# Optimization experiments

Measured on AMD Instinct MI355X. Metric: run time of the kernel, lower is better.

## Reference

```python
import jax, jax.numpy as jnp
import numpy as np

B, S, H, NH, L, ML = 4, 2048, 768, 8, 128, 15
DH = H // NH
PERIOD = 16  # newline every 16 tokens -> 15 content tokens per line


def _layernorm(x, g, b, eps=1e-5):
    m = x.mean(-1, keepdims=True)
    v = ((x - m) ** 2).mean(-1, keepdims=True)
    return (x - m) / jnp.sqrt(v + eps) * g + b


def setup_inputs() -> dict:
    key = jax.random.key(0)
    ks = jax.random.split(key, 8)
    sc = 0.02
    return {
        "hidden": jax.random.normal(ks[0], (B, S, H), jnp.float32),
        "in_proj_w": jax.random.normal(ks[1], (3 * H, H), jnp.float32) * sc,
        "in_proj_b": jnp.zeros((3 * H,), jnp.float32),
        "out_proj_w": jax.random.normal(ks[2], (H, H), jnp.float32) * sc,
        "out_proj_b": jnp.zeros((H,), jnp.float32),
        "W1": jax.random.normal(ks[3], (H, 2 * H), jnp.float32) * sc,
        "b1": jnp.zeros((H,), jnp.float32),
        "g1": jnp.ones((H,), jnp.float32),
        "be1": jnp.zeros((H,), jnp.float32),
        "W2": jax.random.normal(ks[4], (H, H), jnp.float32) * sc,
        "b2": jnp.zeros((H,), jnp.float32),
        "g2": jnp.ones((H,), jnp.float32),
        "be2": jnp.zeros((H,), jnp.float32),
        "W3": jax.random.normal(ks[5], (1, H), jnp.float32) * sc,
        "b3": jnp.zeros((1,), jnp.float32),
        # padded ragged line structure (what the torch loops derive from newline positions)
        "line_starts": jnp.tile(jnp.arange(L, dtype=jnp.int32) * PERIOD, (B, 1)),  # [B,L]
        "line_lens": jnp.full((B, L), ML, jnp.int32),                              # [B,L]
        "context_len": jnp.full((B,), S, jnp.int32),                               # [B]
    }


def reference(hidden, in_proj_w, in_proj_b, out_proj_w, out_proj_b,
              W1, b1, g1, be1, W2, b2, g2, be2, W3, b3,
              line_starts, line_lens, context_len):
    # --- gather per-line tokens into a padded [B, L, ML, H] block ---
    pos = line_starts[:, :, None] + jnp.arange(ML, dtype=line_starts.dtype)      # [B,L,ML]
    tok_mask = jnp.arange(ML)[None, None, :] < line_lens[:, :, None]             # [B,L,ML]
    pos_c = jnp.clip(pos, 0, S - 1)
    bidx = jnp.arange(B)[:, None, None]
    line_tok = hidden[bidx, pos_c]                                               # [B,L,ML,H]

    # --- nn.MultiheadAttention: query=line tokens, key/value=global context ---
    Wq, Wk, Wv = jnp.split(in_proj_w, 3, axis=0)
    bq, bk, bv = jnp.split(in_proj_b, 3, axis=0)
    q = (line_tok @ Wq.T + bq).reshape(B, L, ML, NH, DH)
    k = (hidden @ Wk.T + bk).reshape(B, S, NH, DH)
    v = (hidden @ Wv.T + bv).reshape(B, S, NH, DH)

    scale = 1.0 / np.float32(np.sqrt(DH))
    scores = jnp.einsum('blmhd,bshd->blhms', q, k) * scale                       # [B,L,NH,ML,S]
    kmask = jnp.arange(S)[None, :] < context_len[:, None]                        # [B,S]
    scores = jnp.where(kmask[:, None, None, None, :], scores, -1e9)
    attn = jax.nn.softmax(scores, axis=-1)
    o = jnp.einsum('blhms,bshd->blmhd', attn, v).reshape(B, L, ML, H)
    o = o @ out_proj_w.T + out_proj_b                                            # [B,L,ML,H]

    # --- masked mean-pool over the line's tokens ---
    m = tok_mask[..., None].astype(hidden.dtype)
    denom = jnp.maximum(line_lens, 1)[..., None].astype(hidden.dtype)            # [B,L,1]
    line_mean = (line_tok * m).sum(2) / denom                                    # [B,L,H]
    attn_mean = (o * m).sum(2) / denom                                           # [B,L,H]

    # --- classifier: Linear -> LN -> GELU -> Residual(Linear->LN->GELU) -> Linear ---
    x = jnp.concatenate([line_mean, attn_mean], axis=-1)                         # [B,L,2H]
    x = jax.nn.gelu(_layernorm(x @ W1.T + b1, g1, be1), approximate=False)
    x = x + jax.nn.gelu(_layernorm(x @ W2.T + b2, g2, be2), approximate=False)
    logits = (x @ W3.T + b3)[..., 0]                                             # [B,L]

    # empty lines get logit -10 (as in the torch loop)
    logits = jnp.where(line_lens > 0, logits, jnp.asarray(-10.0, logits.dtype))
    return jax.nn.sigmoid(logits)
```

## Files before the change

### kernel.cpp

```cpp
#include <hip/hip_runtime.h>
#include <hip/hip_bf16.h>
#include <cmath>

using bf16 = __hip_bfloat16;
typedef __attribute__((ext_vector_type(8))) short short8;
typedef __attribute__((ext_vector_type(4))) short s16x4;
typedef __attribute__((ext_vector_type(4))) float f32x4;

#define B_   4
#define S_   2048
#define H_   768
#define H2_  1536
#define H3_  2304
#define NH_  8
#define DH_  96
#define L_   128
#define ML_  15
#define LG_  8
#define QR_  128
#define CH_  32
#define NS_  2
#define SLC_ (S_ / NS_)
#define ELD  36
#define VTLD 40
#define KLD  104
#define VTR  112

__device__ __forceinline__ float gelu_exact(float v) {
    return 0.5f * v * (1.0f + erff(v * 0.7071067811865475f));
}
__device__ __forceinline__ short f2bs(float f) {
    bf16 h = __float2bfloat16(f);
    return *reinterpret_cast<short*>(&h);
}
__device__ __forceinline__ short8 ld_frag8(const short* p) {
    union { short8 v; s16x4 h[2]; } u;
    u.h[0] = *(const s16x4*)p;
    u.h[1] = *(const s16x4*)(p + 4);
    return u.v;
}

__global__ __launch_bounds__(256) void f2b_k(
    const float* __restrict__ src, bf16* __restrict__ dst, int n)
{
    const int i = (blockIdx.x * 256 + threadIdx.x) * 8;
    if (i >= n) return;
    float4 a = *(const float4*)(src + i);
    float4 b = *(const float4*)(src + i + 4);
    short8 r;
    r[0] = f2bs(a.x); r[1] = f2bs(a.y); r[2] = f2bs(a.z); r[3] = f2bs(a.w);
    r[4] = f2bs(b.x); r[5] = f2bs(b.y); r[6] = f2bs(b.z); r[7] = f2bs(b.w);
    *(short8*)(dst + i) = r;
}

template <typename T>
__device__ __forceinline__ void stage8(const T* src, bf16* dst);
template <>
__device__ __forceinline__ void stage8<bf16>(const bf16* src, bf16* dst) {
    *(int4*)dst = *(const int4*)src;
}
template <>
__device__ __forceinline__ void stage8<float>(const float* src, bf16* dst) {
    float4 a = *(const float4*)src;
    float4 b = *(const float4*)(src + 4);
    short8 r;
    r[0] = f2bs(a.x); r[1] = f2bs(a.y); r[2] = f2bs(a.z); r[3] = f2bs(a.w);
    r[4] = f2bs(b.x); r[5] = f2bs(b.y); r[6] = f2bs(b.z); r[7] = f2bs(b.w);
    *(short8*)dst = r;
}

__global__ __launch_bounds__(256) void gemm128_qkv(
    const bf16* __restrict__ A, const bf16* __restrict__ Bm,
    const float* __restrict__ bias, bf16* __restrict__ qk,
    bf16* __restrict__ vt, int M, int K)
{
    __shared__ alignas(16) bf16 As[128 * 32];
    __shared__ alignas(16) bf16 Bs[128 * 32];
    const int t = threadIdx.x;
    const int wave = t >> 6, lane = t & 63;
    const int l15 = lane & 15, quad = lane >> 4;
    const int m0 = blockIdx.x * 128, n0 = blockIdx.y * 128;
    const int wm = wave & 1, wn = wave >> 1;
    const int srow = t >> 1, scol = (t & 1) * 16;

    const bf16* aP = A + (size_t)(m0 + srow) * K + scol;
    const bf16* bP = Bm + (size_t)(n0 + srow) * K + scol;
    bf16* aL = &As[srow * 32 + scol];
    bf16* bL = &Bs[srow * 32 + scol];

    f32x4 acc[4][4];
#pragma unroll
    for (int i = 0; i < 4; i++)
#pragma unroll
        for (int j = 0; j < 4; j++) acc[i][j] = (f32x4){0.f, 0.f, 0.f, 0.f};

    for (int k0 = 0; k0 < K; k0 += 32) {
        int4 ra0 = *(const int4*)(aP + k0);
        int4 ra1 = *(const int4*)(aP + k0 + 8);
        int4 rb0 = *(const int4*)(bP + k0);
        int4 rb1 = *(const int4*)(bP + k0 + 8);
        __syncthreads();
        *(int4*)aL = ra0; *(int4*)(aL + 8) = ra1;
        *(int4*)bL = rb0; *(int4*)(bL + 8) = rb1;
        __syncthreads();
        short8 af[4], bfq[4];
#pragma unroll
        for (int i = 0; i < 4; i++)
            af[i] = *(const short8*)&As[(wm * 64 + i * 16 + l15) * 32 + quad * 8];
#pragma unroll
        for (int j = 0; j < 4; j++)
            bfq[j] = *(const short8*)&Bs[(wn * 64 + j * 16 + l15) * 32 + quad * 8];
#pragma unroll
        for (int i = 0; i < 4; i++)
#pragma unroll
            for (int j = 0; j < 4; j++)
                acc[i][j] = __builtin_amdgcn_mfma_f32_16x16x32_bf16(af[i], bfq[j], acc[i][j], 0, 0, 0);
    }

    if (n0 < H2_) {
#pragma unroll
        for (int j = 0; j < 4; j++) {
            const int col = n0 + wn * 64 + j * 16 + l15;
            const float bv = bias[col];
#pragma unroll
            for (int i = 0; i < 4; i++) {
                const int row = m0 + wm * 64 + i * 16 + quad * 4;
#pragma unroll
                for (int r = 0; r < 4; r++)
                    qk[(size_t)(row + r) * H2_ + col] = __float2bfloat16(acc[i][j][r] + bv);
            }
        }
    } else {
#pragma unroll
        for (int j = 0; j < 4; j++) {
            const int col = n0 + wn * 64 + j * 16 + l15;
            const float bv = bias[col];
            const int dfull = col - H2_;
            const int hh = dfull / DH_, d = dfull - hh * DH_;
#pragma unroll
            for (int i = 0; i < 4; i++) {
                const int row = m0 + wm * 64 + i * 16 + quad * 4;
                const int b = row >> 11, s = row & (S_ - 1);
                s16x4 pk;
#pragma unroll
                for (int r = 0; r < 4; r++) pk[r] = f2bs(acc[i][j][r] + bv);
                *(s16x4*)&vt[((size_t)(b * NH_ + hh) * DH_ + d) * S_ + s] = pk;
            }
        }
    }
}

template <typename TA, typename TB, bool OUT_BF16>
__global__ __launch_bounds__(256) void gemm_bt(
    const TA* __restrict__ A, const TB* __restrict__ Bm,
    const float* __restrict__ bias, void* __restrict__ Cout,
    int M, int N, int K, int ldc, int coff)
{
    __shared__ alignas(16) bf16 As[64 * 32];
    __shared__ alignas(16) bf16 Bs[64 * 32];
    const int t = threadIdx.x;
    const int wave = t >> 6, lane = t & 63;
    const int l15 = lane & 15, quad = lane >> 4;
    const int m0 = blockIdx.x * 64, n0 = blockIdx.y * 64;
    const int srow = t >> 2, schk = (t & 3) * 8;

    const TA* aPtr = A + (size_t)(m0 + srow) * K + schk;
    const TB* bPtr = Bm + (size_t)(n0 + srow) * K + schk;

    f32x4 acc[4] = {{0.f,0.f,0.f,0.f},{0.f,0.f,0.f,0.f},
                    {0.f,0.f,0.f,0.f},{0.f,0.f,0.f,0.f}};
    const int aoff = (wave * 16 + l15) * 32 + quad * 8;

    for (int k0 = 0; k0 < K; k0 += 32) {
        __syncthreads();
        stage8<TA>(aPtr + k0, &As[srow * 32 + schk]);
        stage8<TB>(bPtr + k0, &Bs[srow * 32 + schk]);
        __syncthreads();
        short8 af = *(const short8*)&As[aoff];
#pragma unroll
        for (int nt = 0; nt < 4; nt++) {
            short8 bfr = *(const short8*)&Bs[(nt * 16 + l15) * 32 + quad * 8];
            acc[nt] = __builtin_amdgcn_mfma_f32_16x16x32_bf16(af, bfr, acc[nt], 0, 0, 0);
        }
    }

#pragma unroll
    for (int nt = 0; nt < 4; nt++) {
        int col = n0 + nt * 16 + l15;
        float bv = bias[col];
#pragma unroll
        for (int r = 0; r < 4; r++) {
            int row = m0 + wave * 16 + quad * 4 + r;
            float v = acc[nt][r] + bv;
            if (OUT_BF16) ((bf16*)Cout)[(size_t)row * ldc + coff + col] = __float2bfloat16(v);
            else          ((float*)Cout)[(size_t)row * ldc + coff + col] = v;
        }
    }
}

__global__ __launch_bounds__(256) void attn_slice(
    const bf16* __restrict__ qk, const bf16* __restrict__ vtg,
    const int* __restrict__ line_starts, const int* __restrict__ line_lens,
    const int* __restrict__ context_len,
    bf16* __restrict__ Opart, float* __restrict__ Dpart)
{
    __shared__ alignas(16) union {
        short Qs[QR_ * KLD];
        struct {
            short Ks[CH_ * KLD];
            short Vt[VTR * VTLD];
            short Es[QR_ * ELD];
        } s;
    } U;

    const int t = threadIdx.x;
    const int idx = blockIdx.x;
    const int slice = blockIdx.y;
    const int lg = idx & 15;
    const int bh = idx >> 4;
    const int h = bh & 7, b = bh >> 3;
    const int ctx = context_len[b];
    const int wave = t >> 6, lane = t & 63;
    const int l15 = lane & 15, quad = lane >> 4;

    for (int ii = t; ii < QR_ * 12; ii += 256) {
        const int r = ii / 12, ck = ii - r * 12;
        int4 val; val.x = val.y = val.z = val.w = 0;
        if (r < LG_ * ML_) {
            const int li = r / ML_, m = r - li * ML_;
            const int line = lg * LG_ + li;
            const int len = line_lens[b * L_ + line];
            if (m < len) {
                int sPos = line_starts[b * L_ + line] + m;
                sPos = min(max(sPos, 0), S_ - 1);
                val = *(const int4*)(qk + (size_t)(b * S_ + sPos) * H2_ + h * DH_ + ck * 8);
            }
        }
        *(int4*)&U.Qs[r * KLD + ck * 8] = val;
    }
    __syncthreads();

    short8 qf[2][3];
#pragma unroll
    for (int st = 0; st < 2; st++)
#pragma unroll
        for (int kf = 0; kf < 3; kf++)
            qf[st][kf] = *(const short8*)(U.Qs + ((wave + 4 * st) * 16 + l15) * KLD + kf * 32 + quad * 8);
    __syncthreads();

    f32x4 Oacc[2][7];
#pragma unroll
    for (int st = 0; st < 2; st++)
#pragma unroll
        for (int nt = 0; nt < 7; nt++) Oacc[st][nt] = (f32x4){0.f, 0.f, 0.f, 0.f};

    const float scale = 0.10206207261596577f;
    const size_t kbase = (size_t)b * S_ * H2_ + H_ + h * DH_;
    const size_t vbase = (size_t)(b * NH_ + h) * DH_ * S_;
    const int cbase = slice * SLC_;

    const int k0r = t / 12,        k0c = t - k0r * 12;
    const int k1r = (256 + t) / 12, k1c = (256 + t) - k1r * 12;
    const int v0d = t >> 2,        v0s = (t & 3) * 8;
    const int v1d = (256 + t) >> 2, v1s = ((256 + t) & 3) * 8;
    const int on_r = t >> 4, on_c = t & 15;

    int4 rk0, rk1, rv0, rv1;
    {
        rk0 = *(const int4*)(qk + kbase + (size_t)(cbase + k0r) * H2_ + k0c * 8);
        rv0 = *(const int4*)(vtg + vbase + (size_t)v0d * S_ + cbase + v0s);
        if (t < 128) {
            rk1 = *(const int4*)(qk + kbase + (size_t)(cbase + k1r) * H2_ + k1c * 8);
            rv1 = *(const int4*)(vtg + vbase + (size_t)v1d * S_ + cbase + v1s);
        }
    }

    for (int ci = 0; ci < SLC_ / CH_; ci++) {
        const int c0 = cbase + ci * CH_;
        __syncthreads();
        *(int4*)&U.s.Ks[k0r * KLD + k0c * 8] = rk0;
        *(int4*)&U.s.Vt[v0d * VTLD + v0s] = rv0;
        if (t < 128) {
            *(int4*)&U.s.Ks[k1r * KLD + k1c * 8] = rk1;
            *(int4*)&U.s.Vt[v1d * VTLD + v1s] = rv1;
        }
        {
            unsigned int lo = (c0 + 2 * on_c)     < ctx ? 0x3f80u : 0u;
            unsigned int hi = (c0 + 2 * on_c + 1) < ctx ? 0x3f80u : 0u;
            ((unsigned int*)&U.s.Vt[(96 + on_r) * VTLD])[on_c] = lo | (hi << 16);
        }
        __syncthreads();

        if (ci + 1 < SLC_ / CH_) {
            const int cn = c0 + CH_;
            rk0 = *(const int4*)(qk + kbase + (size_t)(cn + k0r) * H2_ + k0c * 8);
            rv0 = *(const int4*)(vtg + vbase + (size_t)v0d * S_ + cn + v0s);
            if (t < 128) {
                rk1 = *(const int4*)(qk + kbase + (size_t)(cn + k1r) * H2_ + k1c * 8);
                rv1 = *(const int4*)(vtg + vbase + (size_t)v1d * S_ + cn + v1s);
            }
        }

        f32x4 acc[2][2] = {{{0.f,0.f,0.f,0.f},{0.f,0.f,0.f,0.f}},
                           {{0.f,0.f,0.f,0.f},{0.f,0.f,0.f,0.f}}};
#pragma unroll
        for (int ns = 0; ns < 2; ns++)
#pragma unroll
            for (int kf = 0; kf < 3; kf++) {
                short8 kfr = *(const short8*)(U.s.Ks + (ns * 16 + l15) * KLD + kf * 32 + quad * 8);
                acc[0][ns] = __builtin_amdgcn_mfma_f32_16x16x32_bf16(kfr, qf[0][kf], acc[0][ns], 0, 0, 0);
                acc[1][ns] = __builtin_amdgcn_mfma_f32_16x16x32_bf16(kfr, qf[1][kf], acc[1][ns], 0, 0, 0);
            }

#pragma unroll
        for (int st = 0; st < 2; st++)
#pragma unroll
            for (int ns = 0; ns < 2; ns++) {
                s16x4 wv;
#pragma unroll
                for (int r = 0; r < 4; r++) {
                    const int s = c0 + ns * 16 + quad * 4 + r;
                    float e = (s < ctx) ? __expf(acc[st][ns][r] * scale) : 0.f;
                    wv[r] = f2bs(e);
                }
                *(s16x4*)&U.s.Es[((wave + 4 * st) * 16 + l15) * ELD + ns * 16 + quad * 4] = wv;
            }

        short8 pf0 = ld_frag8(U.s.Es + (wave * 16 + l15) * ELD + quad * 8);
        short8 pf1 = ld_frag8(U.s.Es + ((wave + 4) * 16 + l15) * ELD + quad * 8);
#pragma unroll
        for (int nt = 0; nt < 7; nt++) {
            short8 vfr = *(const short8*)&U.s.Vt[(nt * 16 + l15) * VTLD + quad * 8];
            Oacc[0][nt] = __builtin_amdgcn_mfma_f32_16x16x32_bf16(pf0, vfr, Oacc[0][nt], 0, 0, 0);
            Oacc[1][nt] = __builtin_amdgcn_mfma_f32_16x16x32_bf16(pf1, vfr, Oacc[1][nt], 0, 0, 0);
        }
    }

    const size_t pb = (size_t)(slice * 512 + idx) * QR_;
#pragma unroll
    for (int st = 0; st < 2; st++)
#pragma unroll
        for (int r = 0; r < 4; r++) {
            const int row = (wave + 4 * st) * 16 + quad * 4 + r;
#pragma unroll
            for (int nt = 0; nt < 6; nt++)
                Opart[(pb + row) * DH_ + nt * 16 + l15] = __float2bfloat16(Oacc[st][nt][r]);
            if (l15 == 0) Dpart[pb + row] = Oacc[st][6][r];
        }
}

__global__ __launch_bounds__(256) void combine_pool(
    const bf16* __restrict__ Opart, const float* __restrict__ Dpart,
    const int* __restrict__ line_lens, bf16* __restrict__ opool)
{
    __shared__ float invd[LG_ * ML_];
    __shared__ int lens_s[LG_];
    const int idx = blockIdx.x;
    const int lg = idx & 15, bh = idx >> 4;
    const int h = bh & 7, b = bh >> 3;
    const int t = threadIdx.x;
    if (t < LG_) lens_s[t] = line_lens[b * L_ + lg * LG_ + t];
    if (t < LG_ * ML_) {
        float ds = 0.f;
#pragma unroll
        for (int s = 0; s < NS_; s++)
            ds += Dpart[(size_t)(s * 512 + idx) * QR_ + t];
        invd[t] = ds > 0.f ? 1.f / ds : 0.f;
    }
    __syncthreads();
    for (int q = t; q < LG_ * DH_; q += 256) {
        const int li = q / DH_, d = q - li * DH_;
        const int mm = min(lens_s[li], ML_);
        float acc = 0.f;
        for (int m = 0; m < mm; m++) {
            const int row = li * ML_ + m;
            float o = 0.f;
#pragma unroll
            for (int s = 0; s < NS_; s++)
                o += __bfloat162float(Opart[((size_t)(s * 512 + idx) * QR_ + row) * DH_ + d]);
            acc += o * invd[row];
        }
        const int line = lg * LG_ + li;
        opool[(size_t)(b * L_ + line) * H_ + h * DH_ + d] =
            __float2bfloat16(acc / (float)max(lens_s[li], 1));
    }
}

__global__ __launch_bounds__(256) void line_mean_k(
    const bf16* __restrict__ hidden, const int* __restrict__ line_starts,
    const int* __restrict__ line_lens, bf16* __restrict__ x)
{
    const int blk = blockIdx.x;
    const int b = blk >> 7, line = blk & 127;
    const int len = line_lens[b * L_ + line];
    const int start = line_starts[b * L_ + line];
    const int mm = min(len, ML_);
    const float inv = 1.f / (float)max(len, 1);
    for (int d = threadIdx.x; d < H_; d += 256) {
        float s = 0.f;
        for (int m = 0; m < mm; m++) {
            int sp = min(max(start + m, 0), S_ - 1);
            s += __bfloat162float(hidden[(size_t)(b * S_ + sp) * H_ + d]);
        }
        x[(size_t)blk * H2_ + d] = __float2bfloat16(s * inv);
    }
}

__global__ __launch_bounds__(256) void ln_gelu_k(
    const float* __restrict__ hin, const float* __restrict__ g,
    const float* __restrict__ be, float* __restrict__ uout, bf16* __restrict__ ubf)
{
    __shared__ float red[16];
    const int row = blockIdx.x, t = threadIdx.x;
    const float* hr = hin + (size_t)row * H_;
    float v[3];
    float s1 = 0.f, s2 = 0.f;
#pragma unroll
    for (int k = 0; k < 3; k++) {
        v[k] = hr[t + k * 256];
        s1 += v[k]; s2 += v[k] * v[k];
    }
#pragma unroll
    for (int m = 1; m < 64; m <<= 1) { s1 += __shfl_xor(s1, m, 64); s2 += __shfl_xor(s2, m, 64); }
    const int wave = t >> 6, lane = t & 63;
    if (lane == 0) { red[wave] = s1; red[8 + wave] = s2; }
    __syncthreads();
    s1 = red[0] + red[1] + red[2] + red[3];
    s2 = red[8] + red[9] + red[10] + red[11];
    const float mean = s1 * (1.f / H_);
    const float var = s2 * (1.f / H_) - mean * mean;
    const float rstd = 1.f / sqrtf(var + 1e-5f);
#pragma unroll
    for (int k = 0; k < 3; k++) {
        const int d = t + k * 256;
        float y = (v[k] - mean) * rstd * g[d] + be[d];
        y = gelu_exact(y);
        uout[(size_t)row * H_ + d] = y;
        ubf[(size_t)row * H_ + d] = __float2bfloat16(y);
    }
}

__global__ __launch_bounds__(256) void final_k(
    const float* __restrict__ h2, const float* __restrict__ u,
    const float* __restrict__ g2, const float* __restrict__ be2,
    const float* __restrict__ W3, const float* __restrict__ b3,
    const int* __restrict__ line_lens, float* __restrict__ out)
{
    __shared__ float red[16];
    const int row = blockIdx.x, t = threadIdx.x;
    const float* hr = h2 + (size_t)row * H_;
    float v[3];
    float s1 = 0.f, s2 = 0.f;
#pragma unroll
    for (int k = 0; k < 3; k++) {
        v[k] = hr[t + k * 256];
        s1 += v[k]; s2 += v[k] * v[k];
    }
#pragma unroll
    for (int m = 1; m < 64; m <<= 1) { s1 += __shfl_xor(s1, m, 64); s2 += __shfl_xor(s2, m, 64); }
    const int wave = t >> 6, lane = t & 63;
    if (lane == 0) { red[wave] = s1; red[8 + wave] = s2; }
    __syncthreads();
    s1 = red[0] + red[1] + red[2] + red[3];
    s2 = red[8] + red[9] + red[10] + red[11];
    const float mean = s1 * (1.f / H_);
    const float var = s2 * (1.f / H_) - mean * mean;
    const float rstd = 1.f / sqrtf(var + 1e-5f);
    float dotp = 0.f;
#pragma unroll
    for (int k = 0; k < 3; k++) {
        const int d = t + k * 256;
        float y = (v[k] - mean) * rstd * g2[d] + be2[d];
        y = u[(size_t)row * H_ + d] + gelu_exact(y);
        dotp += y * W3[d];
    }
#pragma unroll
    for (int m = 1; m < 64; m <<= 1) dotp += __shfl_xor(dotp, m, 64);
    __syncthreads();
    if (lane == 0) red[wave] = dotp;
    __syncthreads();
    if (t == 0) {
        float logit = red[0] + red[1] + red[2] + red[3] + b3[0];
        if (line_lens[row] <= 0) logit = -10.f;
        out[row] = 1.f / (1.f + __expf(-logit));
    }
}

extern "C" void kernel_launch(void* const* d_in, const int* in_sizes, int n_in,
                              void* d_out, int out_size, void* d_ws, size_t ws_size,
                              hipStream_t stream)
{
    const float* hidden     = (const float*)d_in[0];
    const float* in_proj_w  = (const float*)d_in[1];
    const float* in_proj_b  = (const float*)d_in[2];
    const float* out_proj_w = (const float*)d_in[3];
    const float* out_proj_b = (const float*)d_in[4];
    const float* W1         = (const float*)d_in[5];
    const float* b1         = (const float*)d_in[6];
    const float* g1         = (const float*)d_in[7];
    const float* be1        = (const float*)d_in[8];
    const float* W2         = (const float*)d_in[9];
    const float* b2         = (const float*)d_in[10];
    const float* g2         = (const float*)d_in[11];
    const float* be2        = (const float*)d_in[12];
    const float* W3         = (const float*)d_in[13];
    const float* b3         = (const float*)d_in[14];
    const int* line_starts  = (const int*)d_in[15];
    const int* line_lens    = (const int*)d_in[16];
    const int* context_len  = (const int*)d_in[17];

    const int BL = B_ * L_;
    const size_t nh = (size_t)B_ * S_ * H_;
    const size_t nw = (size_t)H3_ * H_;
    const size_t opart_n = (size_t)NS_ * 512 * QR_ * DH_;

    char* w = (char*)d_ws;
    bf16* qk    = (bf16*)w;  w += (size_t)B_ * S_ * H2_ * sizeof(bf16);
    bf16* vtg   = (bf16*)w;  w += (size_t)B_ * NH_ * DH_ * S_ * sizeof(bf16);
    char* ovl = w;
    bf16* hb    = (bf16*)ovl;
    bf16* wqkvb = (bf16*)(ovl + nh * sizeof(bf16));
    bf16* Opart = (bf16*)ovl;
    w = ovl + opart_n * sizeof(bf16);
    float* Dpart = (float*)w; w += (size_t)NS_ * 512 * QR_ * sizeof(float);
    bf16* opool = (bf16*)w;  w += (size_t)BL * H_ * sizeof(bf16);
    bf16* x     = (bf16*)w;  w += (size_t)BL * H2_ * sizeof(bf16);
    float* h1   = (float*)w; w += (size_t)BL * H_ * sizeof(float);
    float* uu   = (float*)w; w += (size_t)BL * H_ * sizeof(float);
    bf16* ubf   = (bf16*)w;  w += (size_t)BL * H_ * sizeof(bf16);
    float* h2   = (float*)w; w += (size_t)BL * H_ * sizeof(float);

    f2b_k<<<(int)(nh / (256 * 8)), 256, 0, stream>>>(hidden, hb, (int)nh);
    f2b_k<<<(int)(nw / (256 * 8)), 256, 0, stream>>>(in_proj_w, wqkvb, (int)nw);

    gemm128_qkv<<<dim3(B_ * S_ / 128, H3_ / 128), 256, 0, stream>>>(
        hb, wqkvb, in_proj_b, qk, vtg, B_ * S_, H_);
    line_mean_k<<<BL, 256, 0, stream>>>(hb, line_starts, line_lens, x);
    attn_slice<<<dim3(512, NS_), 256, 0, stream>>>(
        qk, vtg, line_starts, line_lens, context_len, Opart, Dpart);
    combine_pool<<<512, 256, 0, stream>>>(Opart, Dpart, line_lens, opool);
    gemm_bt<bf16, float, true><<<dim3(BL / 64, H_ / 64), 256, 0, stream>>>(
        opool, out_proj_w, out_proj_b, x, BL, H_, H_, H2_, H_);
    gemm_bt<bf16, float, false><<<dim3(BL / 64, H_ / 64), 256, 0, stream>>>(
        x, W1, b1, h1, BL, H_, H2_, H_, 0);
    ln_gelu_k<<<BL, 256, 0, stream>>>(h1, g1, be1, uu, ubf);
    gemm_bt<bf16, float, false><<<dim3(BL / 64, H_ / 64), 256, 0, stream>>>(
        ubf, W2, b2, h2, BL, H_, H_, H_, 0);
    final_k<<<BL, 256, 0, stream>>>(h2, uu, g2, be2, W3, b3, line_lens, (float*)d_out);
}
```

Before: 348.3 us.

## Load QKV GEMM tiles via direct global-to-LDS loads and raise split count

The QKV projection GEMM now stages A and B tiles with global_load_lds (16-byte direct global-to-LDS transfers) instead of loading into registers and then storing to shared memory. The wave-to-row mapping is rearranged so each wave fills contiguous 16-row blocks of 512 elements. Separately, the sequence split count NS_ goes from 2 to 4, giving the attention stage more parallel slices at the cost of more partial results to combine. The direct-LDS path frees registers and skips the store instructions, but the loop still uses a single buffer with two barriers per step. It also relies on the __syncthreads after the load to cover completion of the asynchronous transfers.

```diff
diff --git a/kernel.cpp b/kernel.cpp
--- a/kernel.cpp
+++ b/kernel.cpp
@@ -19,7 +19,7 @@
 #define LG_  8
 #define QR_  128
 #define CH_  32
-#define NS_  2
+#define NS_  4
 #define SLC_ (S_ / NS_)
 #define ELD  36
 #define VTLD 40
@@ -38,6 +38,11 @@
     u.h[0] = *(const s16x4*)p;
     u.h[1] = *(const s16x4*)(p + 4);
     return u.v;
+}
+__device__ __forceinline__ void gl_lds16(const bf16* g, bf16* l) {
+    __builtin_amdgcn_global_load_lds(
+        (const __attribute__((address_space(1))) unsigned int*)g,
+        (__attribute__((address_space(3))) unsigned int*)l, 16, 0, 0);
 }
 
 __global__ __launch_bounds__(256) void f2b_k(
@@ -81,12 +86,18 @@
     const int l15 = lane & 15, quad = lane >> 4;
     const int m0 = blockIdx.x * 128, n0 = blockIdx.y * 128;
     const int wm = wave & 1, wn = wave >> 1;
-    const int srow = t >> 1, scol = (t & 1) * 16;
-
-    const bf16* aP = A + (size_t)(m0 + srow) * K + scol;
-    const bf16* bP = Bm + (size_t)(n0 + srow) * K + scol;
-    bf16* aL = &As[srow * 32 + scol];
-    bf16* bL = &Bs[srow * 32 + scol];
+
+    const int r0s = (wave * 2 + 0) * 16 + (lane >> 2);
+    const int r1s = (wave * 2 + 1) * 16 + (lane >> 2);
+    const int segc = (lane & 3) * 8;
+    const bf16* gA0 = A + (size_t)(m0 + r0s) * K + segc;
+    const bf16* gA1 = A + (size_t)(m0 + r1s) * K + segc;
+    const bf16* gB0 = Bm + (size_t)(n0 + r0s) * K + segc;
+    const bf16* gB1 = Bm + (size_t)(n0 + r1s) * K + segc;
+    bf16* lA0 = As + (wave * 2 + 0) * 512;
+    bf16* lA1 = As + (wave * 2 + 1) * 512;
+    bf16* lB0 = Bs + (wave * 2 + 0) * 512;
+    bf16* lB1 = Bs + (wave * 2 + 1) * 512;
 
     f32x4 acc[4][4];
 #pragma unroll
@@ -95,13 +106,11 @@
         for (int j = 0; j < 4; j++) acc[i][j] = (f32x4){0.f, 0.f, 0.f, 0.f};
 
     for (int k0 = 0; k0 < K; k0 += 32) {
-        int4 ra0 = *(const int4*)(aP + k0);
-        int4 ra1 = *(const int4*)(aP + k0 + 8);
-        int4 rb0 = *(const int4*)(bP + k0);
-        int4 rb1 = *(const int4*)(bP + k0 + 8);
         __syncthreads();
-        *(int4*)aL = ra0; *(int4*)(aL + 8) = ra1;
-        *(int4*)bL = rb0; *(int4*)(bL + 8) = rb1;
+        gl_lds16(gA0 + k0, lA0);
+        gl_lds16(gA1 + k0, lA1);
+        gl_lds16(gB0 + k0, lB0);
+        gl_lds16(gB1 + k0, lB1);
         __syncthreads();
         short8 af[4], bfq[4];
 #pragma unroll
```

After: 377.5 us. 8.4% more time.
